# Kernel optimization log

Hardware: AMD Instinct MI355X
Metric: run time of the kernel (lower is better)

## Reference

```python
import jax, jax.numpy as jnp
import numpy as np

N, DIM, L = 65536, 128, 8


def setup_inputs() -> dict:
    rng = np.random.default_rng(0)
    # depth-consistent random tree: node 0 is root (depth 0); every other node
    # gets depth in [1, L-1] and a parent chosen uniformly among depth-1 nodes.
    depth = np.zeros(N, dtype=np.int64)
    depth[1:] = rng.integers(1, L, size=N - 1)
    depth = np.sort(depth)  # node 0 stays root; contiguous levels
    parent = np.full(N, N, dtype=np.int64)  # sentinel N for the root (dropped in segment_sum slice)
    for d in range(1, L):
        cur = np.nonzero(depth == d)[0]
        prev = np.nonzero(depth == d - 1)[0]
        parent[cur] = rng.choice(prev, size=cur.size)
    key = jax.random.key(0)
    k = jax.random.split(key, 5)
    s = 1.0 / np.sqrt(DIM)
    return {
        "x": jax.random.normal(k[0], (N, DIM), jnp.float32),
        "parent": jnp.asarray(parent),
        "depth": jnp.asarray(depth),
        "Wioux": jax.random.normal(k[1], (DIM, 3 * DIM), jnp.float32) * s,
        "Wiouh": jax.random.normal(k[2], (DIM, 3 * DIM), jnp.float32) * s,
        "Wfx": jax.random.normal(k[3], (DIM, DIM), jnp.float32) * s,
        "Wfh": jax.random.normal(k[4], (DIM, DIM), jnp.float32) * s,
        "n_levels": L,
    }


def reference(x, parent, depth, Wioux, Wiouh, Wfx, Wfh, n_levels):
    n, dim = x.shape
    xi = x @ Wioux          # [N, 3d]  precomputed input projections
    xf = x @ Wfx            # [N, d]
    pidx = jnp.minimum(parent, n - 1)  # safe gather index (root sentinel clipped; root is never a child)
    h = jnp.zeros_like(x)
    c = jnp.zeros_like(x)
    # process tree bottom-up, one depth level at a time (equivalent to the
    # torch depth-descending per-node loop since children are exactly one level deeper)
    for d in range(int(n_levels) - 1, -1, -1):
        child = depth == d + 1          # nodes that are children of level-d nodes
        cm = child[:, None]
        h_sum = jax.ops.segment_sum(jnp.where(cm, h, 0.0), parent, num_segments=n + 1)[:n]
        n_child = jax.ops.segment_sum(child.astype(x.dtype), parent, num_segments=n + 1)[:n]
        # per-child forget gate: sigmoid(fx(x[parent]) + fh(h_child))
        f = jax.nn.sigmoid(xf[pidx] + h @ Wfh)
        fc_sum = jax.ops.segment_sum(jnp.where(cm, f * c, 0.0), parent, num_segments=n + 1)[:n]
        i_, o_, u_ = jnp.split(xi + h_sum @ Wiouh, 3, axis=-1)
        c_int = fc_sum + jax.nn.sigmoid(i_) * jnp.tanh(u_)
        h_int = jax.nn.sigmoid(o_) * jnp.tanh(c_int)
        leaf = (n_child == 0)[:, None]  # leaves: h = x, c = tanh(x) (as in torch code)
        h_new = jnp.where(leaf, x, h_int)
        c_new = jnp.where(leaf, jnp.tanh(x), c_int)
        lvl = (depth == d)[:, None]
        h = jnp.where(lvl, h_new, h)
        c = jnp.where(lvl, c_new, c)
    return h
```

## Files before the change

### kernel.cpp

```cpp
#include <hip/hip_runtime.h>
#include <hip/hip_bf16.h>

#define DIM 128
#define LVL 8

typedef unsigned int u32;
typedef unsigned short u16;

using bf16x8 = __attribute__((ext_vector_type(8))) short;
using f32x4  = __attribute__((ext_vector_type(4))) float;

__device__ __forceinline__ float bf2f(u16 u) { union { u32 i; float f; } v; v.i = ((u32)u) << 16; return v.f; }
__device__ __forceinline__ u16 f2bf(float f) { __hip_bfloat16 b = __float2bfloat16(f); return *reinterpret_cast<u16*>(&b); }
__device__ __forceinline__ u32 pk2(float lo, float hi) { return (u32)f2bf(lo) | ((u32)f2bf(hi) << 16); }
__device__ __forceinline__ float sigf(float x) { return 1.f / (1.f + __expf(-x)); }
__device__ __forceinline__ float tanhfast(float x) { return 1.f - 2.f / (__expf(2.f * x) + 1.f); }

__global__ void k_levels(const int* __restrict__ depth, int n, int* __restrict__ ofs, int* __restrict__ deg) {
  int d = threadIdx.x;
  if (d <= LVL) {
    int lo = 0, hi = n;
    while (lo < hi) { int mid = (lo + hi) >> 1; if (depth[mid] < d) lo = mid + 1; else hi = mid; }
    ofs[d] = lo;
  }
  __syncthreads();
  if (d == 0) deg[0] = ofs[2] - ofs[1];
}

__global__ void k_mark(const int* __restrict__ parent, const int* __restrict__ depth, int n,
                       int* __restrict__ deg) {
  int j = blockIdx.x * blockDim.x + threadIdx.x;
  if (j >= n) return;
  if (depth[j] < 2) return;
  int p = parent[j];
  if (p >= 0 && p < n) atomicAdd(&deg[p], 1);
}

__global__ void k_compact(const int* __restrict__ depth, const int* __restrict__ deg,
                          const int* __restrict__ ofs, int n,
                          int* __restrict__ lcnt, int* __restrict__ plist) {
  __shared__ int lcount[8];
  __shared__ int lbase[8];
  int tid = threadIdx.x;
  if (tid < 8) lcount[tid] = 0;
  __syncthreads();
  int j = blockIdx.x * 256 + tid;
  bool ok = (j < n) && (j > 0) && (deg[j] != 0);
  int d = 0, slot = 0;
  if (ok) {
    d = depth[j];
    slot = atomicAdd(&lcount[d], 1);
  }
  __syncthreads();
  if (tid < 8 && lcount[tid] > 0)
    lbase[tid] = atomicAdd(&lcnt[tid], lcount[tid]);
  __syncthreads();
  if (ok) plist[ofs[d] + lbase[d] + slot] = j;
}

__global__ void k_zero(const int* __restrict__ deg, int n, float* __restrict__ hsum, float* __restrict__ fcsum) {
  int row = blockIdx.x * 4 + (threadIdx.x >> 6);
  if (row >= n) return;
  if (deg[row] < 2) return;
  int l = threadIdx.x & 63;
  float2 z; z.x = 0.f; z.y = 0.f;
  *(float2*)(hsum + (size_t)row * DIM + l * 2) = z;
  *(float2*)(fcsum + (size_t)row * DIM + l * 2) = z;
}

__global__ void k_prep(const float* __restrict__ Wioux, const float* __restrict__ Wiouh,
                       const float* __restrict__ Wfx, const float* __restrict__ Wfh,
                       u16* __restrict__ WcT, u16* __restrict__ WallIou, u16* __restrict__ WfhTp) {
  int i = blockIdx.x * 256 + threadIdx.x;
  if (i >= 1152 * 128) return;
  int c = i >> 7, k = i & 127;
  if (c < 640) {
    float v;
    if (c < 384)      v = Wioux[(size_t)k * 384 + c];
    else if (c < 512) v = Wfx[(size_t)k * 128 + (c - 384)];
    else              v = Wfh[(size_t)k * 128 + (c - 512)];
    WcT[(size_t)c * 128 + k] = f2bf(v);
  } else if (c < 1024) {
    int cc = c - 640;
    int kp = (k & 7) * 16 + (k >> 3);
    WallIou[(size_t)cc * 128 + (k ^ ((cc & 7) << 3))] = f2bf(Wiouh[(size_t)kp * 384 + cc]);
  } else {
    int cc = c - 1024;
    int kp = (k & 7) * 16 + (k >> 3);
    WfhTp[(size_t)cc * 128 + k] = f2bf(Wfh[(size_t)kp * 128 + cc]);
  }
}

__global__ __launch_bounds__(256) void k_big(const float* __restrict__ x, const u16* __restrict__ WcT,
                                             const int* __restrict__ deg, u16* __restrict__ xi,
                                             u16* __restrict__ xfh, int n) {
  __shared__ __align__(16) char smem[16384 + 32768];
  char* xsb = smem;
  char* wtb = smem + 16384;
  __shared__ int flg[64];
  __shared__ int s_anyP, s_anyL;
  int tid = threadIdx.x;
  int wave = tid >> 6, lane = tid & 63, m = lane & 15, kg = lane >> 4;
  int row0 = blockIdx.x * 64;
  if (row0 >= n) return;
  if (tid < 64) flg[tid] = (row0 + tid < n) ? ((deg[row0 + tid] > 0) ? 1 : 2) : 0;
  __syncthreads();
  if (tid == 0) {
    int ap = 0, al = 0;
    for (int r = 0; r < 64; ++r) { ap |= (flg[r] == 1); al |= (flg[r] == 2); }
    s_anyP = ap; s_anyL = al;
  }
  for (int i = tid; i < 64 * 16; i += 256) {
    int r = i >> 4, c8 = (i & 15) * 8;
    int gr = row0 + r;
    uint4 o = make_uint4(0u, 0u, 0u, 0u);
    if (gr < n) {
      float4 a = *(const float4*)(x + (size_t)gr * DIM + c8);
      float4 b = *(const float4*)(x + (size_t)gr * DIM + c8 + 4);
      o = make_uint4(pk2(a.x, a.y), pk2(a.z, a.w), pk2(b.x, b.y), pk2(b.z, b.w));
    }
    *(uint4*)(xsb + r * 256 + ((c8 * 2) ^ ((r & 7) << 4))) = o;
  }
  int arow = wave * 16 + m;
  for (int ci = 0; ci < 5; ++ci) {
    __syncthreads();
    bool need = (ci < 4) ? (s_anyP != 0) : (s_anyL != 0);
    if (!need) continue;
    for (int i = tid; i < 128 * 16; i += 256) {
      int cl = i >> 4, k8 = (i & 15) * 8;
      uint4 v = *(const uint4*)(WcT + (size_t)(ci * 128 + cl) * 128 + k8);
      *(uint4*)(wtb + cl * 256 + ((k8 * 2) ^ ((cl & 7) << 4))) = v;
    }
    __syncthreads();
    f32x4 acc[8];
    #pragma unroll
    for (int nt = 0; nt < 8; ++nt) acc[nt] = (f32x4){0.f, 0.f, 0.f, 0.f};
    #pragma unroll
    for (int kk = 0; kk < 4; ++kk) {
      int kbyte = kk * 64 + kg * 16;
      bf16x8 a = *(const bf16x8*)(xsb + arow * 256 + (kbyte ^ ((arow & 7) << 4)));
      #pragma unroll
      for (int nt = 0; nt < 8; ++nt) {
        int col = nt * 16 + m;
        bf16x8 b = *(const bf16x8*)(wtb + col * 256 + (kbyte ^ ((col & 7) << 4)));
        acc[nt] = __builtin_amdgcn_mfma_f32_16x16x32_bf16(a, b, acc[nt], 0, 0, 0);
      }
    }
    #pragma unroll
    for (int r = 0; r < 4; ++r) {
      int rl = wave * 16 + kg * 4 + r;
      int gr = row0 + rl;
      if (gr < n) {
        uint4 o = make_uint4(pk2(acc[0][r], acc[1][r]), pk2(acc[2][r], acc[3][r]),
                             pk2(acc[4][r], acc[5][r]), pk2(acc[6][r], acc[7][r]));
        if (ci < 4) { if (flg[rl] == 1) *(uint4*)(xi + ((size_t)gr * 4 + ci) * 128 + m * 8) = o; }
        else        { if (flg[rl] == 2) *(uint4*)(xfh + (size_t)gr * DIM + m * 8) = o; }
      }
    }
  }
}

__global__ __launch_bounds__(256) void k_leaf(
    const float* __restrict__ x, const u16* __restrict__ xfh, const u16* __restrict__ xi,
    const int* __restrict__ deg, const int* __restrict__ parent, const int* __restrict__ ofs,
    float* __restrict__ hout, float* hsum, float* fcsum, int n) {
  __shared__ float redh[128], redf[128];
  __shared__ int s_l1;
  int tid = threadIdx.x;
  if (tid < 128) { redh[tid] = 0.f; redf[tid] = 0.f; }
  if (tid == 0) s_l1 = 0;
  __syncthreads();
  int row = blockIdx.x * 64 + (tid >> 2);
  int qq = tid & 3;
  int o1 = ofs[1], o2 = ofs[2];
  bool work = (row < n) && (row > 0) && (deg[row] == 0);
  bool isl1 = false;
  if (work) {
    int p = parent[row];
    int dg = deg[p];
    isl1 = (row >= o1) && (row < o2);
    const u16* xf = xi + ((size_t)p * 4 + 3) * 128;
    const u16* xh = xfh + (size_t)row * DIM;
    #pragma unroll 2
    for (int c4 = 0; c4 < 32; c4 += 4) {
      int col0 = qq * 32 + c4;
      float4 xv4 = *(const float4*)(x + (size_t)row * DIM + col0);
      *(float4*)(hout + (size_t)row * DIM + col0) = xv4;
      #pragma unroll
      for (int e = 0; e < 4; ++e) {
        int col = col0 + e;
        int idx = (col & 15) * 8 + (col >> 4);
        float xv = ((const float*)&xv4)[e];
        float fcv = sigf(bf2f(xf[idx]) + bf2f(xh[idx])) * tanhfast(xv);
        if (isl1) {
          atomicAdd(&redh[idx], xv);
          atomicAdd(&redf[idx], fcv);
        } else if (dg == 1) {
          hsum[(size_t)p * DIM + idx] = xv;
          fcsum[(size_t)p * DIM + idx] = fcv;
        } else {
          atomicAdd(&hsum[(size_t)p * DIM + idx], xv);
          atomicAdd(&fcsum[(size_t)p * DIM + idx], fcv);
        }
      }
    }
  }
  if (isl1 && qq == 0) s_l1 = 1;
  __syncthreads();
  if (s_l1 && tid < 128) {
    atomicAdd(&hsum[tid], redh[tid]);
    atomicAdd(&fcsum[tid], redf[tid]);
  }
}

__global__ __launch_bounds__(256) void k_level(
    const u16* __restrict__ WallIou, const u16* __restrict__ WfhTp, const u16* __restrict__ xi,
    const int* __restrict__ deg, const int* __restrict__ parent,
    const int* __restrict__ ofs, const int* __restrict__ lcnt, const int* __restrict__ plist,
    float* __restrict__ hout, float* hsum, float* fcsum, int d) {
  __shared__ __align__(16) char wl[98304];
  __shared__ __align__(16) char hsball[16384];
  __shared__ float redh[128], redf[128];
  int cnt = lcnt[d];
  if ((int)blockIdx.x * 64 >= cnt) return;
  int tid = threadIdx.x;
  int wid = tid >> 6, lane = tid & 63, m = lane & 15, kg = lane >> 4;
  char* hsb = hsball + wid * 4096;
  for (int i = tid; i < 6144; i += 256) ((uint4*)wl)[i] = ((const uint4*)WallIou)[i];
  if (tid < 128) { redh[tid] = 0.f; redf[tid] = 0.f; }
  int base = ofs[d];
  __syncthreads();

  for (int tb = blockIdx.x; tb * 64 < cnt; tb += (int)gridDim.x) {
    int t = tb * 4 + wid;
    int idv = -1;
    if (lane < 16) {
      int s = t * 16 + lane;
      if (s < cnt) idv = plist[base + s];
    }
    int pv = (lane < 16 && idv >= 0) ? parent[idv] : 0;
    int dgv = (lane < 16 && idv >= 0) ? deg[pv] : 0;
    int idr[4], prr[4], dgr[4];
    #pragma unroll
    for (int r = 0; r < 4; ++r) {
      idr[r] = __shfl(idv, kg * 4 + r, 64);
      prr[r] = __shfl(pv,  kg * 4 + r, 64);
      dgr[r] = __shfl(dgv, kg * 4 + r, 64);
    }
    int id_m = __shfl(idv, m, 64);

    bf16x8 afr[4];
    #pragma unroll
    for (int kk = 0; kk < 4; ++kk) {
      union { u32 u[4]; bf16x8 v; } cu;
      cu.u[0] = cu.u[1] = cu.u[2] = cu.u[3] = 0u;
      if (id_m >= 0) {
        const float* hp = hsum + (size_t)id_m * DIM + kk * 32 + kg * 8;
        float4 a = *(const float4*)hp; float4 b = *(const float4*)(hp + 4);
        cu.u[0] = pk2(a.x, a.y); cu.u[1] = pk2(a.z, a.w);
        cu.u[2] = pk2(b.x, b.y); cu.u[3] = pk2(b.z, b.w);
      }
      afr[kk] = cu.v;
    }

    float P[8][4], O[8][4];
    const int cxs[3] = {0, 2, 1};
    #pragma unroll
    for (int phx = 0; phx < 3; ++phx) {
      int cx = cxs[phx];
      f32x4 acc[8];
      #pragma unroll
      for (int nt = 0; nt < 8; ++nt) acc[nt] = (f32x4){0.f, 0.f, 0.f, 0.f};
      #pragma unroll
      for (int kk = 0; kk < 4; ++kk) {
        int kby = kk * 64 + kg * 16;
        #pragma unroll
        for (int nt = 0; nt < 8; ++nt) {
          int brow = cx * 128 + nt * 16 + m;
          bf16x8 b = *(const bf16x8*)(wl + brow * 256 + (kby ^ ((brow & 7) << 4)));
          acc[nt] = __builtin_amdgcn_mfma_f32_16x16x32_bf16(afr[kk], b, acc[nt], 0, 0, 0);
        }
      }
      #pragma unroll
      for (int r = 0; r < 4; ++r) {
        int gc = idr[r] >= 0 ? idr[r] : 0;
        uint4 q = *(const uint4*)(xi + ((size_t)gc * 4 + cx) * 128 + m * 8);
        #pragma unroll
        for (int nt = 0; nt < 8; ++nt) {
          float tt = bf2f(((const u16*)&q)[nt]) + acc[nt][r];
          if (phx == 0)      P[nt][r] = sigf(tt);
          else if (phx == 1) P[nt][r] *= tanhfast(tt);
          else               O[nt][r] = sigf(tt);
        }
      }
    }

    float hv[8][4], cv[8][4];
    #pragma unroll
    for (int r = 0; r < 4; ++r) {
      int rl = kg * 4 + r;
      int id = idr[r];
      int gc = id >= 0 ? id : 0;
      float4 fa = *(const float4*)(fcsum + (size_t)gc * DIM + m * 8);
      float4 fb = *(const float4*)(fcsum + (size_t)gc * DIM + m * 8 + 4);
      #pragma unroll
      for (int nt = 0; nt < 8; ++nt) {
        float fcv = (nt < 4) ? ((const float*)&fa)[nt] : ((const float*)&fb)[nt - 4];
        float c_ = fcv + P[nt][r];
        float h_ = O[nt][r] * tanhfast(c_);
        if (id < 0) { c_ = 0.f; h_ = 0.f; }
        cv[nt][r] = c_; hv[nt][r] = h_;
        if (id >= 0) hout[(size_t)id * DIM + nt * 16 + m] = h_;
      }
      uint4 o = make_uint4(pk2(hv[0][r], hv[1][r]), pk2(hv[2][r], hv[3][r]),
                           pk2(hv[4][r], hv[5][r]), pk2(hv[6][r], hv[7][r]));
      *(uint4*)(hsb + rl * 256 + ((m * 16) ^ ((rl & 7) << 4))) = o;
    }

    f32x4 fp[8];
    #pragma unroll
    for (int nt = 0; nt < 8; ++nt) fp[nt] = (f32x4){0.f, 0.f, 0.f, 0.f};
    #pragma unroll
    for (int kk = 0; kk < 4; ++kk) {
      int kby = kk * 64 + kg * 16;
      bf16x8 a = *(const bf16x8*)(hsb + m * 256 + (kby ^ ((m & 7) << 4)));
      #pragma unroll
      for (int nt = 0; nt < 8; ++nt) {
        bf16x8 b = *(const bf16x8*)(WfhTp + (size_t)(nt * 16 + m) * 128 + kk * 32 + kg * 8);
        fp[nt] = __builtin_amdgcn_mfma_f32_16x16x32_bf16(a, b, fp[nt], 0, 0, 0);
      }
    }

    if (d == 1) {
      uint4 qf = *(const uint4*)(xi + (size_t)3 * 128 + m * 8);
      float th[8], tf[8];
      #pragma unroll
      for (int nt = 0; nt < 8; ++nt) {
        float sh = 0.f, sf = 0.f;
        #pragma unroll
        for (int r = 0; r < 4; ++r) {
          sh += hv[nt][r];
          sf += (idr[r] >= 0) ? sigf(bf2f(((const u16*)&qf)[nt]) + fp[nt][r]) * cv[nt][r] : 0.f;
        }
        th[nt] = sh; tf[nt] = sf;
      }
      #pragma unroll
      for (int nt = 0; nt < 8; ++nt) {
        th[nt] += __shfl_xor(th[nt], 16, 64); th[nt] += __shfl_xor(th[nt], 32, 64);
        tf[nt] += __shfl_xor(tf[nt], 16, 64); tf[nt] += __shfl_xor(tf[nt], 32, 64);
      }
      if (kg == 0) {
        #pragma unroll
        for (int nt = 0; nt < 8; ++nt) {
          atomicAdd(&redh[m * 8 + nt], th[nt]);
          atomicAdd(&redf[m * 8 + nt], tf[nt]);
        }
      }
    } else {
      #pragma unroll
      for (int r = 0; r < 4; ++r) {
        int id = idr[r];
        if (id < 0) continue;
        int p = prr[r];
        uint4 qf = *(const uint4*)(xi + ((size_t)p * 4 + 3) * 128 + m * 8);
        float fc[8];
        #pragma unroll
        for (int nt = 0; nt < 8; ++nt)
          fc[nt] = sigf(bf2f(((const u16*)&qf)[nt]) + fp[nt][r]) * cv[nt][r];
        if (dgr[r] == 1) {
          *(float4*)(hsum  + (size_t)p * DIM + m * 8)     = make_float4(hv[0][r], hv[1][r], hv[2][r], hv[3][r]);
          *(float4*)(hsum  + (size_t)p * DIM + m * 8 + 4) = make_float4(hv[4][r], hv[5][r], hv[6][r], hv[7][r]);
          *(float4*)(fcsum + (size_t)p * DIM + m * 8)     = make_float4(fc[0], fc[1], fc[2], fc[3]);
          *(float4*)(fcsum + (size_t)p * DIM + m * 8 + 4) = make_float4(fc[4], fc[5], fc[6], fc[7]);
        } else {
          #pragma unroll
          for (int nt = 0; nt < 8; ++nt) {
            atomicAdd(hsum  + (size_t)p * DIM + m * 8 + nt, hv[nt][r]);
            atomicAdd(fcsum + (size_t)p * DIM + m * 8 + nt, fc[nt]);
          }
        }
      }
    }
  }
  if (d == 1) {
    __syncthreads();
    if (tid < 128) {
      atomicAdd(&hsum[tid], redh[tid]);
      atomicAdd(&fcsum[tid], redf[tid]);
    }
  }
}

__global__ void k_root(const float* __restrict__ x, const float* __restrict__ Wiouh,
                       const u16* __restrict__ xi, const int* __restrict__ deg,
                       const float* __restrict__ hsum, const float* __restrict__ fcsum,
                       float* __restrict__ hout) {
  __shared__ float hsn[128];
  __shared__ float pre[384];
  int tid = threadIdx.x;
  if (deg[0] == 0) { if (tid < 128) hout[tid] = x[tid]; return; }
  if (tid < 128) {
    int kp = (tid & 7) * 16 + (tid >> 3);
    hsn[kp] = hsum[tid];
  }
  __syncthreads();
  float a = 0.f;
  #pragma unroll 4
  for (int k = 0; k < 128; ++k) a += hsn[k] * Wiouh[(size_t)k * 384 + tid];
  pre[tid] = a;
  __syncthreads();
  if (tid < 128) {
    int j = tid;
    int c = (j & 7) * 16 + (j >> 3);
    float iv = bf2f(xi[0 * 128 + j]) + pre[c];
    float ov = bf2f(xi[1 * 128 + j]) + pre[128 + c];
    float uv = bf2f(xi[2 * 128 + j]) + pre[256 + c];
    float ci_ = fcsum[j] + sigf(iv) * tanhfast(uv);
    hout[c] = sigf(ov) * tanhfast(ci_);
  }
}

extern "C" void kernel_launch(void* const* d_in, const int* in_sizes, int n_in,
                              void* d_out, int out_size, void* d_ws, size_t ws_size,
                              hipStream_t stream) {
  const float* x    = (const float*)d_in[0];
  const int* parent = (const int*)d_in[1];
  const int* depth  = (const int*)d_in[2];
  const float* Wioux = (const float*)d_in[3];
  const float* Wiouh = (const float*)d_in[4];
  const float* Wfx   = (const float*)d_in[5];
  const float* Wfh   = (const float*)d_in[6];
  int n = in_sizes[0] / DIM;
  float* h = (float*)d_out;

  u16*   WcT     = (u16*)d_ws;
  u16*   WallIou = WcT + 640 * 128;
  u16*   WfhTp   = WallIou + 384 * 128;
  u16*   xi      = WfhTp + 128 * 128;
  u16*   xfh     = xi + (size_t)n * 512;
  float* hsum    = (float*)(xfh + (size_t)n * DIM);
  float* fcsum   = hsum + (size_t)n * DIM;
  int*   deg     = (int*)(fcsum + (size_t)n * DIM);
  int*   lcnt    = deg + n;
  int*   ofs     = lcnt + 8;
  int*   plist   = ofs + (LVL + 1);

  hipMemsetAsync(deg, 0, (size_t)(n + 8) * sizeof(int), stream);
  k_prep<<<576, 256, 0, stream>>>(Wioux, Wiouh, Wfx, Wfh, WcT, WallIou, WfhTp);
  k_levels<<<1, 32, 0, stream>>>(depth, n, ofs, deg);
  k_mark<<<(n + 255) / 256, 256, 0, stream>>>(parent, depth, n, deg);
  k_compact<<<(n + 255) / 256, 256, 0, stream>>>(depth, deg, ofs, n, lcnt, plist);
  k_zero<<<(n + 3) / 4, 256, 0, stream>>>(deg, n, hsum, fcsum);
  k_big<<<(n + 63) / 64, 256, 0, stream>>>(x, WcT, deg, xi, xfh, n);
  k_leaf<<<(n + 63) / 64, 256, 0, stream>>>(x, xfh, xi, deg, parent, ofs, h, hsum, fcsum, n);

  for (int d = LVL - 2; d >= 1; --d)
    k_level<<<147, 256, 0, stream>>>(WallIou, WfhTp, xi, deg, parent, ofs, lcnt, plist,
                                     h, hsum, fcsum, d);
  k_root<<<1, 384, 0, stream>>>(x, Wiouh, xi, deg, hsum, fcsum, h);
}
```

Measured before the change: 443.4 us.

## Fuse per-level kernels into one persistent kernel with grid barrier

Replaces the six per-level k_level launches with a single persistent k_tree kernel of 160 blocks that loops over levels and uses a global atomic counter barrier between them. Wfh is now packed into the swizzled shared-memory weight array alongside Wiouh, so the forget-gate GEMM reads from LDS instead of global memory. k_leaf is also reorganised to 8 threads per row with vector loads and stores. This removes launch gaps and the repeated weight loads per level, at the cost of a spin barrier that relies on all 160 blocks being co-resident (1 block per CU with 128KB+ LDS).

```diff
diff --git a/kernel.cpp b/kernel.cpp
--- a/kernel.cpp
+++ b/kernel.cpp
@@ -3,6 +3,7 @@
 
 #define DIM 128
 #define LVL 8
+#define NB 160
 
 typedef unsigned int u32;
 typedef unsigned short u16;
@@ -70,7 +71,7 @@
 
 __global__ void k_prep(const float* __restrict__ Wioux, const float* __restrict__ Wiouh,
                        const float* __restrict__ Wfx, const float* __restrict__ Wfh,
-                       u16* __restrict__ WcT, u16* __restrict__ WallIou, u16* __restrict__ WfhTp) {
+                       u16* __restrict__ WcT, u16* __restrict__ Wall) {
   int i = blockIdx.x * 256 + threadIdx.x;
   if (i >= 1152 * 128) return;
   int c = i >> 7, k = i & 127;
@@ -80,14 +81,11 @@
     else if (c < 512) v = Wfx[(size_t)k * 128 + (c - 384)];
     else              v = Wfh[(size_t)k * 128 + (c - 512)];
     WcT[(size_t)c * 128 + k] = f2bf(v);
-  } else if (c < 1024) {
+  } else {
     int cc = c - 640;
     int kp = (k & 7) * 16 + (k >> 3);
-    WallIou[(size_t)cc * 128 + (k ^ ((cc & 7) << 3))] = f2bf(Wiouh[(size_t)kp * 384 + cc]);
-  } else {
-    int cc = c - 1024;
-    int kp = (k & 7) * 16 + (k >> 3);
-    WfhTp[(size_t)cc * 128 + k] = f2bf(Wfh[(size_t)kp * 128 + cc]);
+    float v = (cc < 384) ? Wiouh[(size_t)kp * 384 + cc] : Wfh[(size_t)kp * 128 + (cc - 384)];
+    Wall[(size_t)cc * 128 + (k ^ ((cc & 7) << 3))] = f2bf(v);
   }
 }
 
@@ -170,8 +168,8 @@
   if (tid < 128) { redh[tid] = 0.f; redf[tid] = 0.f; }
   if (tid == 0) s_l1 = 0;
   __syncthreads();
-  int row = blockIdx.x * 64 + (tid >> 2);
-  int qq = tid & 3;
+  int row = blockIdx.x * 32 + (tid >> 3);
+  int q = tid & 7;
   int o1 = ofs[1], o2 = ofs[2];
   bool work = (row < n) && (row > 0) && (deg[row] == 0);
   bool isl1 = false;
@@ -179,33 +177,46 @@
     int p = parent[row];
     int dg = deg[p];
     isl1 = (row >= o1) && (row < o2);
-    const u16* xf = xi + ((size_t)p * 4 + 3) * 128;
-    const u16* xh = xfh + (size_t)row * DIM;
-    #pragma unroll 2
-    for (int c4 = 0; c4 < 32; c4 += 4) {
-      int col0 = qq * 32 + c4;
-      float4 xv4 = *(const float4*)(x + (size_t)row * DIM + col0);
-      *(float4*)(hout + (size_t)row * DIM + col0) = xv4;
-      #pragma unroll
-      for (int e = 0; e < 4; ++e) {
-        int col = col0 + e;
-        int idx = (col & 15) * 8 + (col >> 4);
-        float xv = ((const float*)&xv4)[e];
-        float fcv = sigf(bf2f(xf[idx]) + bf2f(xh[idx])) * tanhfast(xv);
-        if (isl1) {
-          atomicAdd(&redh[idx], xv);
-          atomicAdd(&redf[idx], fcv);
-        } else if (dg == 1) {
-          hsum[(size_t)p * DIM + idx] = xv;
-          fcsum[(size_t)p * DIM + idx] = fcv;
-        } else {
-          atomicAdd(&hsum[(size_t)p * DIM + idx], xv);
-          atomicAdd(&fcsum[(size_t)p * DIM + idx], fcv);
-        }
-      }
-    }
-  }
-  if (isl1 && qq == 0) s_l1 = 1;
+    float hvv[16], fcc[16];
+    #pragma unroll
+    for (int g = 0; g < 8; ++g) {
+      float2 xv2 = *(const float2*)(x + (size_t)row * DIM + g * 16 + q * 2);
+      hvv[g] = xv2.x; hvv[g + 8] = xv2.y;
+      *(float2*)(hout + (size_t)row * DIM + g * 16 + q * 2) = xv2;
+    }
+    const u16* xf = xi + ((size_t)p * 4 + 3) * 128 + q * 16;
+    const u16* xh = xfh + (size_t)row * DIM + q * 16;
+    uint4 a0 = *(const uint4*)xf, a1 = *(const uint4*)(xf + 8);
+    uint4 b0 = *(const uint4*)xh, b1 = *(const uint4*)(xh + 8);
+    const u16* fa0 = (const u16*)&a0; const u16* fa1 = (const u16*)&a1;
+    const u16* hb0 = (const u16*)&b0; const u16* hb1 = (const u16*)&b1;
+    #pragma unroll
+    for (int t = 0; t < 16; ++t) {
+      u16 xfv = (t < 8) ? fa0[t] : fa1[t - 8];
+      u16 xhv = (t < 8) ? hb0[t] : hb1[t - 8];
+      fcc[t] = sigf(bf2f(xfv) + bf2f(xhv)) * tanhfast(hvv[t]);
+    }
+    if (isl1) {
+      #pragma unroll
+      for (int t = 0; t < 16; ++t) {
+        atomicAdd(&redh[q * 16 + t], hvv[t]);
+        atomicAdd(&redf[q * 16 + t], fcc[t]);
+      }
+    } else if (dg == 1) {
+      #pragma unroll
+      for (int t = 0; t < 16; t += 4) {
+        *(float4*)(hsum  + (size_t)p * DIM + q * 16 + t) = make_float4(hvv[t], hvv[t+1], hvv[t+2], hvv[t+3]);
+        *(float4*)(fcsum + (size_t)p * DIM + q * 16 + t) = make_float4(fcc[t], fcc[t+1], fcc[t+2], fcc[t+3]);
+      }
+    } else {
+      #pragma unroll
+      for (int t = 0; t < 16; ++t) {
+        atomicAdd(hsum  + (size_t)p * DIM + q * 16 + t, hvv[t]);
+        atomicAdd(fcsum + (size_t)p * DIM + q * 16 + t, fcc[t]);
+      }
+    }
+  }
+  if (isl1 && q == 0) s_l1 = 1;
   __syncthreads();
   if (s_l1 && tid < 128) {
     atomicAdd(&hsum[tid], redh[tid]);
@@ -213,180 +224,195 @@
   }
 }
 
-__global__ __launch_bounds__(256) void k_level(
-    const u16* __restrict__ WallIou, const u16* __restrict__ WfhTp, const u16* __restrict__ xi,
+__global__ __launch_bounds__(256, 1) void k_tree(
+    const u16* __restrict__ Wall, const u16* __restrict__ xi,
     const int* __restrict__ deg, const int* __restrict__ parent,
     const int* __restrict__ ofs, const int* __restrict__ lcnt, const int* __restrict__ plist,
-    float* __restrict__ hout, float* hsum, float* fcsum, int d) {
-  __shared__ __align__(16) char wl[98304];
+    float* __restrict__ hout, float* hsum, float* fcsum, int* bar) {
+  __shared__ __align__(16) char wl[131072];
   __shared__ __align__(16) char hsball[16384];
   __shared__ float redh[128], redf[128];
-  int cnt = lcnt[d];
-  if ((int)blockIdx.x * 64 >= cnt) return;
-  int tid = threadIdx.x;
+  __shared__ int s_hasl1;
+  int tid = threadIdx.x, bid = blockIdx.x;
   int wid = tid >> 6, lane = tid & 63, m = lane & 15, kg = lane >> 4;
   char* hsb = hsball + wid * 4096;
-  for (int i = tid; i < 6144; i += 256) ((uint4*)wl)[i] = ((const uint4*)WallIou)[i];
+  for (int i = tid; i < 8192; i += 256) ((uint4*)wl)[i] = ((const uint4*)Wall)[i];
   if (tid < 128) { redh[tid] = 0.f; redf[tid] = 0.f; }
-  int base = ofs[d];
-  __syncthreads();
-
-  for (int tb = blockIdx.x; tb * 64 < cnt; tb += (int)gridDim.x) {
-    int t = tb * 4 + wid;
-    int idv = -1;
-    if (lane < 16) {
-      int s = t * 16 + lane;
-      if (s < cnt) idv = plist[base + s];
-    }
-    int pv = (lane < 16 && idv >= 0) ? parent[idv] : 0;
-    int dgv = (lane < 16 && idv >= 0) ? deg[pv] : 0;
-    int idr[4], prr[4], dgr[4];
-    #pragma unroll
-    for (int r = 0; r < 4; ++r) {
-      idr[r] = __shfl(idv, kg * 4 + r, 64);
-      prr[r] = __shfl(pv,  kg * 4 + r, 64);
-      dgr[r] = __shfl(dgv, kg * 4 + r, 64);
-    }
-    int id_m = __shfl(idv, m, 64);
-
-    bf16x8 afr[4];
-    #pragma unroll
-    for (int kk = 0; kk < 4; ++kk) {
-      union { u32 u[4]; bf16x8 v; } cu;
-      cu.u[0] = cu.u[1] = cu.u[2] = cu.u[3] = 0u;
-      if (id_m >= 0) {
-        const float* hp = hsum + (size_t)id_m * DIM + kk * 32 + kg * 8;
-        float4 a = *(const float4*)hp; float4 b = *(const float4*)(hp + 4);
-        cu.u[0] = pk2(a.x, a.y); cu.u[1] = pk2(a.z, a.w);
-        cu.u[2] = pk2(b.x, b.y); cu.u[3] = pk2(b.z, b.w);
-      }
-      afr[kk] = cu.v;
-    }
-
-    float P[8][4], O[8][4];
-    const int cxs[3] = {0, 2, 1};
-    #pragma unroll
-    for (int phx = 0; phx < 3; ++phx) {
-      int cx = cxs[phx];
-      f32x4 acc[8];
-      #pragma unroll
-      for (int nt = 0; nt < 8; ++nt) acc[nt] = (f32x4){0.f, 0.f, 0.f, 0.f};
+  if (tid == 0) s_hasl1 = 0;
+  __syncthreads();
+  int phase = 0;
+  for (int d = 6; d >= 1; --d) {
+    int cnt = lcnt[d], base = ofs[d];
+    for (int t = wid * NB + bid; t * 16 < cnt; t += 4 * NB) {
+      int idv = -1;
+      if (lane < 16) {
+        int s = t * 16 + lane;
+        if (s < cnt) idv = plist[base + s];
+      }
+      int pv = (lane < 16 && idv >= 0) ? parent[idv] : 0;
+      int dgv = (lane < 16 && idv >= 0) ? deg[pv] : 0;
+      int idr[4], prr[4], dgr[4];
+      #pragma unroll
+      for (int r = 0; r < 4; ++r) {
+        idr[r] = __shfl(idv, kg * 4 + r, 64);
+        prr[r] = __shfl(pv,  kg * 4 + r, 64);
+        dgr[r] = __shfl(dgv, kg * 4 + r, 64);
+      }
+      int id_m = __shfl(idv, m, 64);
+
+      bf16x8 afr[4];
+      #pragma unroll
+      for (int kk = 0; kk < 4; ++kk) {
+        union { u32 u[4]; bf16x8 v; } cu;
+        cu.u[0] = cu.u[1] = cu.u[2] = cu.u[3] = 0u;
+        if (id_m >= 0) {
+          const float* hp = hsum + (size_t)id_m * DIM + kk * 32 + kg * 8;
+          float4 a = *(const float4*)hp; float4 b = *(const float4*)(hp + 4);
+          cu.u[0] = pk2(a.x, a.y); cu.u[1] = pk2(a.z, a.w);
+          cu.u[2] = pk2(b.x, b.y); cu.u[3] = pk2(b.z, b.w);
+        }
+        afr[kk] = cu.v;
+      }
+
+      float P[8][4], O[8][4];
+      const int cxs[3] = {0, 2, 1};
+      #pragma unroll
+      for (int phx = 0; phx < 3; ++phx) {
+        int cx = cxs[phx];
+        f32x4 acc[8];
+        #pragma unroll
+        for (int nt = 0; nt < 8; ++nt) acc[nt] = (f32x4){0.f, 0.f, 0.f, 0.f};
+        #pragma unroll
+        for (int kk = 0; kk < 4; ++kk) {
+          int kby = kk * 64 + kg * 16;
+          #pragma unroll
+          for (int nt = 0; nt < 8; ++nt) {
+            int brow = cx * 128 + nt * 16 + m;
+            bf16x8 b = *(const bf16x8*)(wl + brow * 256 + (kby ^ ((brow & 7) << 4)));
+            acc[nt] = __builtin_amdgcn_mfma_f32_16x16x32_bf16(afr[kk], b, acc[nt], 0, 0, 0);
+          }
+        }
+        #pragma unroll
+        for (int r = 0; r < 4; ++r) {
+          int gc = idr[r] >= 0 ? idr[r] : 0;
+          uint4 q = *(const uint4*)(xi + ((size_t)gc * 4 + cx) * 128 + m * 8);
+          #pragma unroll
+          for (int nt = 0; nt < 8; ++nt) {
+            float tt = bf2f(((const u16*)&q)[nt]) + acc[nt][r];
+            if (phx == 0)      P[nt][r] = sigf(tt);
+            else if (phx == 1) P[nt][r] *= tanhfast(tt);
+            else               O[nt][r] = sigf(tt);
+          }
+        }
+      }
+
+      float hv[8][4], cv[8][4];
+      #pragma unroll
+      for (int r = 0; r < 4; ++r) {
+        int rl = kg * 4 + r;
+        int id = idr[r];
+        int gc = id >= 0 ? id : 0;
+        float4 fa = *(const float4*)(fcsum + (size_t)gc * DIM + m * 8);
+        float4 fb = *(const float4*)(fcsum + (size_t)gc * DIM + m * 8 + 4);
+        #pragma unroll
+        for (int nt = 0; nt < 8; ++nt) {
+          float fcv = (nt < 4) ? ((const float*)&fa)[nt] : ((const float*)&fb)[nt - 4];
+          float c_ = fcv + P[nt][r];
+          float h_ = O[nt][r] * tanhfast(c_);
+          if (id < 0) { c_ = 0.f; h_ = 0.f; }
+          cv[nt][r] = c_; hv[nt][r] = h_;
+          if (id >= 0) hout[(size_t)id * DIM + nt * 16 + m] = h_;
+        }
+        uint4 o = make_uint4(pk2(hv[0][r], hv[1][r]), pk2(hv[2][r], hv[3][r]),
+                             pk2(hv[4][r], hv[5][r]), pk2(hv[6][r], hv[7][r]));
+        *(uint4*)(hsb + rl * 256 + ((m * 16) ^ ((rl & 7) << 4))) = o;
+      }
+
+      f32x4 fp[8];
+      #pragma unroll
+      for (int nt = 0; nt < 8; ++nt) fp[nt] = (f32x4){0.f, 0.f, 0.f, 0.f};
       #pragma unroll
       for (int kk = 0; kk < 4; ++kk) {
         int kby = kk * 64 + kg * 16;
+        bf16x8 a = *(const bf16x8*)(hsb + m * 256 + (kby ^ ((m & 7) << 4)));
         #pragma unroll
         for (int nt = 0; nt < 8; ++nt) {
-          int brow = cx * 128 + nt * 16 + m;
+          int brow = 384 + nt * 16 + m;
           bf16x8 b = *(const bf16x8*)(wl + brow * 256 + (kby ^ ((brow & 7) << 4)));
-          acc[nt] = __builtin_amdgcn_mfma_f32_16x16x32_bf16(afr[kk], b, acc[nt], 0, 0, 0);
-        }
-      }
-      #pragma unroll
-      for (int r = 0; r < 4; ++r) {
-        int gc = idr[r] >= 0 ? idr[r] : 0;
-        uint4 q = *(const uint4*)(xi + ((size_t)gc * 4 + cx) * 128 + m * 8);
+          fp[nt] = __builtin_amdgcn_mfma_f32_16x16x32_bf16(a, b, fp[nt], 0, 0, 0);
+        }
+      }
+
+      if (d == 1) {
+        if (lane == 0) s_hasl1 = 1;
+        uint4 qf = *(const uint4*)(xi + (size_t)3 * 128 + m * 8);
+        float th[8], tf[8];
         #pragma unroll
         for (int nt = 0; nt < 8; ++nt) {
-          float tt = bf2f(((const u16*)&q)[nt]) + acc[nt][r];
-          if (phx == 0)      P[nt][r] = sigf(tt);
-          else if (phx == 1) P[nt][r] *= tanhfast(tt);
-          else               O[nt][r] = sigf(tt);
-        }
-      }
-    }
-
-    float hv[8][4], cv[8][4];
-    #pragma unroll
-    for (int r = 0; r < 4; ++r) {
-      int rl = kg * 4 + r;
-      int id = idr[r];
-      int gc = id >= 0 ? id : 0;
-      float4 fa = *(const float4*)(fcsum + (size_t)gc * DIM + m * 8);
-      float4 fb = *(const float4*)(fcsum + (size_t)gc * DIM + m * 8 + 4);
-      #pragma unroll
-      for (int nt = 0; nt < 8; ++nt) {
-        float fcv = (nt < 4) ? ((const float*)&fa)[nt] : ((const float*)&fb)[nt - 4];
-        float c_ = fcv + P[nt][r];
-        float h_ = O[nt][r] * tanhfast(c_);
-        if (id < 0) { c_ = 0.f; h_ = 0.f; }
-        cv[nt][r] = c_; hv[nt][r] = h_;
-        if (id >= 0) hout[(size_t)id * DIM + nt * 16 + m] = h_;
-      }
-      uint4 o = make_uint4(pk2(hv[0][r], hv[1][r]), pk2(hv[2][r], hv[3][r]),
-                           pk2(hv[4][r], hv[5][r]), pk2(hv[6][r], hv[7][r]));
-      *(uint4*)(hsb + rl * 256 + ((m * 16) ^ ((rl & 7) << 4))) = o;
-    }
-
-    f32x4 fp[8];
-    #pragma unroll
-    for (int nt = 0; nt < 8; ++nt) fp[nt] = (f32x4){0.f, 0.f, 0.f, 0.f};
-    #pragma unroll
-    for (int kk = 0; kk < 4; ++kk) {
-      int kby = kk * 64 + kg * 16;
-      bf16x8 a = *(const bf16x8*)(hsb + m * 256 + (kby ^ ((m & 7) << 4)));
-      #pragma unroll
-      for (int nt = 0; nt < 8; ++nt) {
-        bf16x8 b = *(const bf16x8*)(WfhTp + (size_t)(nt * 16 + m) * 128 + kk * 32 + kg * 8);
-        fp[nt] = __builtin_amdgcn_mfma_f32_16x16x32_bf16(a, b, fp[nt], 0, 0, 0);
-      }
-    }
-
-    if (d == 1) {
-      uint4 qf = *(const uint4*)(xi + (size_t)3 * 128 + m * 8);
-      float th[8], tf[8];
-      #pragma unroll
-      for (int nt = 0; nt < 8; ++nt) {
-        float sh = 0.f, sf = 0.f;
-        #pragma unroll
-        for (int r = 0; r < 4; ++r) {
-          sh += hv[nt][r];
-          sf += (idr[r] >= 0) ? sigf(bf2f(((const u16*)&qf)[nt]) + fp[nt][r]) * cv[nt][r] : 0.f;
-        }
-        th[nt] = sh; tf[nt] = sf;
-      }
-      #pragma unroll
-      for (int nt = 0; nt < 8; ++nt) {
-        th[nt] += __shfl_xor(th[nt], 16, 64); th[nt] += __shfl_xor(th[nt], 32, 64);
-        tf[nt] += __shfl_xor(tf[nt], 16, 64); tf[nt] += __shfl_xor(tf[nt], 32, 64);
-      }
-      if (kg == 0) {
+          float sh = 0.f, sf = 0.f;
+          #pragma unroll
+          for (int r = 0; r < 4; ++r) {
+            sh += hv[nt][r];
+            sf += (idr[r] >= 0) ? sigf(bf2f(((const u16*)&qf)[nt]) + fp[nt][r]) * cv[nt][r] : 0.f;
+          }
+          th[nt] = sh; tf[nt] = sf;
+        }
         #pragma unroll
         for (int nt = 0; nt < 8; ++nt) {
-          atomicAdd(&redh[m * 8 + nt], th[nt]);
-          atomicAdd(&redf[m * 8 + nt], tf[nt]);
-        }
-      }
-    } else {
-      #pragma unroll
-      for (int r = 0; r < 4; ++r) {
-        int id = idr[r];
-        if (id < 0) continue;
-        int p = prr[r];
-        uint4 qf = *(const uint4*)(xi + ((size_t)p * 4 + 3) * 128 + m * 8);
-        float fc[8];
-        #pragma unroll
-        for (int nt = 0; nt < 8; ++nt)
-          fc[nt] = sigf(bf2f(((const u16*)&qf)[nt]) + fp[nt][r]) * cv[nt][r];
-        if (dgr[r] == 1) {
-          *(float4*)(hsum  + (size_t)p * DIM + m * 8)     = make_float4(hv[0][r], hv[1][r], hv[2][r], hv[3][r]);
-          *(float4*)(hsum  + (size_t)p * DIM + m * 8 + 4) = make_float4(hv[4][r], hv[5][r], hv[6][r], hv[7][r]);
-          *(float4*)(fcsum + (size_t)p * DIM + m * 8)     = make_float4(fc[0], fc[1], fc[2], fc[3]);
-          *(float4*)(fcsum + (size_t)p * DIM + m * 8 + 4) = make_float4(fc[4], fc[5], fc[6], fc[7]);
-        } else {
+          th[nt] += __shfl_xor(th[nt], 16, 64); th[nt] += __shfl_xor(th[nt], 32, 64);
+          tf[nt] += __shfl_xor(tf[nt], 16, 64); tf[nt] += __shfl_xor(tf[nt], 32, 64);
+        }
+        if (kg == 0) {
           #pragma unroll
           for (int nt = 0; nt < 8; ++nt) {
-            atomicAdd(hsum  + (size_t)p * DIM + m * 8 + nt, hv[nt][r]);
-            atomicAdd(fcsum + (size_t)p * DIM + m * 8 + nt, fc[nt]);
+            atomicAdd(&redh[m * 8 + nt], th[nt]);
+            atomicAdd(&redf[m * 8 + nt], tf[nt]);
           }
         }
-      }
-    }
-  }
-  if (d == 1) {
-    __syncthreads();
-    if (tid < 128) {
-      atomicAdd(&hsum[tid], redh[tid]);
-      atomicAdd(&fcsum[tid], redf[tid]);
+      } else {
+        #pragma unroll
+        for (int r = 0; r < 4; ++r) {
+          int id = idr[r];
+          if (id < 0) continue;
+          int p = prr[r];
+          uint4 qf = *(const uint4*)(xi + ((size_t)p * 4 + 3) * 128 + m * 8);
+          float fc[8];
+          #pragma unroll
+          for (int nt = 0; nt < 8; ++nt)
+            fc[nt] = sigf(bf2f(((const u16*)&qf)[nt]) + fp[nt][r]) * cv[nt][r];
+          if (dgr[r] == 1) {
+            *(float4*)(hsum  + (size_t)p * DIM + m * 8)     = make_float4(hv[0][r], hv[1][r], hv[2][r], hv[3][r]);
+            *(float4*)(hsum  + (size_t)p * DIM + m * 8 + 4) = make_float4(hv[4][r], hv[5][r], hv[6][r], hv[7][r]);
+            *(float4*)(fcsum + (size_t)p * DIM + m * 8)     = make_float4(fc[0], fc[1], fc[2], fc[3]);
+            *(float4*)(fcsum + (size_t)p * DIM + m * 8 + 4) = make_float4(fc[4], fc[5], fc[6], fc[7]);
+          } else {
+            #pragma unroll
+            for (int nt = 0; nt < 8; ++nt) {
+              atomicAdd(hsum  + (size_t)p * DIM + m * 8 + nt, hv[nt][r]);
+              atomicAdd(fcsum + (size_t)p * DIM + m * 8 + nt, fc[nt]);
+            }
+          }
+        }
+      }
+    }
+
+    if (d == 1) {
+      __syncthreads();
+      if (s_hasl1 && tid < 128) {
+        atomicAdd(&hsum[tid], redh[tid]);
+        atomicAdd(&fcsum[tid], redf[tid]);
+      }
+    } else {
+      ++phase;
+      __syncthreads();
+      if (tid == 0) {
+        __threadfence();
+        atomicAdd(bar, 1);
+        int target = phase * NB;
+        while (__hip_atomic_load(bar, __ATOMIC_ACQUIRE, __HIP_MEMORY_SCOPE_AGENT) < target)
+          __builtin_amdgcn_s_sleep(2);
+      }
+      __syncthreads();
     }
   }
 }
@@ -433,29 +459,27 @@
   int n = in_sizes[0] / DIM;
   float* h = (float*)d_out;
 
-  u16*   WcT     = (u16*)d_ws;
-  u16*   WallIou = WcT + 640 * 128;
-  u16*   WfhTp   = WallIou + 384 * 128;
-  u16*   xi      = WfhTp + 128 * 128;
-  u16*   xfh     = xi + (size_t)n * 512;
-  float* hsum    = (float*)(xfh + (size_t)n * DIM);
-  float* fcsum   = hsum + (size_t)n * DIM;
-  int*   deg     = (int*)(fcsum + (size_t)n * DIM);
-  int*   lcnt    = deg + n;
-  int*   ofs     = lcnt + 8;
-  int*   plist   = ofs + (LVL + 1);
-
-  hipMemsetAsync(deg, 0, (size_t)(n + 8) * sizeof(int), stream);
-  k_prep<<<576, 256, 0, stream>>>(Wioux, Wiouh, Wfx, Wfh, WcT, WallIou, WfhTp);
+  u16*   WcT   = (u16*)d_ws;
+  u16*   Wall  = WcT + 640 * 128;
+  u16*   xi    = Wall + 512 * 128;
+  u16*   xfh   = xi + (size_t)n * 512;
+  float* hsum  = (float*)(xfh + (size_t)n * DIM);
+  float* fcsum = hsum + (size_t)n * DIM;
+  int*   deg   = (int*)(fcsum + (size_t)n * DIM);
+  int*   lcnt  = deg + n;
+  int*   bar   = lcnt + 8;
+  int*   ofs   = bar + 8;
+  int*   plist = ofs + (LVL + 1);
+
+  hipMemsetAsync(deg, 0, (size_t)(n + 16) * sizeof(int), stream);
+  k_prep<<<576, 256, 0, stream>>>(Wioux, Wiouh, Wfx, Wfh, WcT, Wall);
   k_levels<<<1, 32, 0, stream>>>(depth, n, ofs, deg);
   k_mark<<<(n + 255) / 256, 256, 0, stream>>>(parent, depth, n, deg);
   k_compact<<<(n + 255) / 256, 256, 0, stream>>>(depth, deg, ofs, n, lcnt, plist);
   k_zero<<<(n + 3) / 4, 256, 0, stream>>>(deg, n, hsum, fcsum);
   k_big<<<(n + 63) / 64, 256, 0, stream>>>(x, WcT, deg, xi, xfh, n);
-  k_leaf<<<(n + 63) / 64, 256, 0, stream>>>(x, xfh, xi, deg, parent, ofs, h, hsum, fcsum, n);
-
-  for (int d = LVL - 2; d >= 1; --d)
-    k_level<<<147, 256, 0, stream>>>(WallIou, WfhTp, xi, deg, parent, ofs, lcnt, plist,
-                                     h, hsum, fcsum, d);
+  k_leaf<<<(n + 31) / 32, 256, 0, stream>>>(x, xfh, xi, deg, parent, ofs, h, hsum, fcsum, n);
+
+  k_tree<<<NB, 256, 0, stream>>>(Wall, xi, deg, parent, ofs, lcnt, plist, h, hsum, fcsum, bar);
   k_root<<<1, 384, 0, stream>>>(x, Wiouh, xi, deg, hsum, fcsum, h);
 }
```

Measured after the change: 651.4 us. 46.9% more time.
